# Performance work log

Measured on AMD Instinct MI355X. Metric: run time of the kernel, lower is better.

Reference implementation:

```python
import jax, jax.numpy as jnp
import numpy as np

B, T, LE = 8, 128, 128
V, VEXT = 32000, 32100
D, H, DFF, MAXLEN = 512, 8, 2048, 512


def _ln(x, g, b, eps=1e-5):
    m = jnp.mean(x, axis=-1, keepdims=True)
    v = jnp.mean((x - m) ** 2, axis=-1, keepdims=True)
    return (x - m) / jnp.sqrt(v + eps) * g + b


def _mha(q_in, k_in, v_in, in_w, in_b, out_w, out_b, mask=None):
    # torch nn.MultiheadAttention (batch_first): packed in_proj [3D, D]
    d = q_in.shape[-1]
    dh = d // H
    wq, wk, wv = in_w[:d], in_w[d:2 * d], in_w[2 * d:]
    bq, bk, bv = in_b[:d], in_b[d:2 * d], in_b[2 * d:]
    q = q_in @ wq.T + bq
    k = k_in @ wk.T + bk
    v = v_in @ wv.T + bv
    def split(x):  # [B, L, D] -> [B, H, L, dh]
        b, l, _ = x.shape
        return x.reshape(b, l, H, dh).transpose(0, 2, 1, 3)
    q, k, v = split(q), split(k), split(v)
    scores = jnp.einsum('bhqd,bhkd->bhqk', q, k) / jnp.sqrt(jnp.asarray(dh, q.dtype))
    if mask is not None:
        scores = scores + mask  # broadcast [T, T] additive mask
    attn = jax.nn.softmax(scores, axis=-1)  # [B, H, Lq, Lk]
    out = jnp.einsum('bhqk,bhkd->bhqd', attn, v)
    b, _, lq, _ = out.shape
    out = out.transpose(0, 2, 1, 3).reshape(b, lq, d)
    return out @ out_w.T + out_b, attn


def setup_inputs() -> dict:
    key = jax.random.key(0)
    ks = jax.random.split(key, 16)
    s = 0.02
    p = lambda i, shape: jax.random.normal(ks[i], shape, jnp.float32) * s
    return {
        'trg_input_ids': jax.random.randint(ks[0], (B, T), 0, V),
        'emofused': jax.random.normal(ks[1], (B, LE, D), jnp.float32),
        'src_token_ids': jax.random.randint(ks[2], (B, LE), 0, VEXT),
        'extended_vocab_size': VEXT,
        'tok_emb': p(3, (V, D)),
        'pos_emb': p(4, (MAXLEN, D)),
        'sa_in_w': p(5, (3 * D, D)), 'sa_in_b': jnp.zeros(3 * D, jnp.float32),
        'sa_out_w': p(6, (D, D)), 'sa_out_b': jnp.zeros(D, jnp.float32),
        'ca_in_w': p(7, (3 * D, D)), 'ca_in_b': jnp.zeros(3 * D, jnp.float32),
        'ca_out_w': p(8, (D, D)), 'ca_out_b': jnp.zeros(D, jnp.float32),
        'w1': p(9, (DFF, D)), 'b1': jnp.zeros(DFF, jnp.float32),
        'w2': p(10, (D, DFF)), 'b2': jnp.zeros(D, jnp.float32),
        'n1_g': jnp.ones(D, jnp.float32), 'n1_b': jnp.zeros(D, jnp.float32),
        'n2_g': jnp.ones(D, jnp.float32), 'n2_b': jnp.zeros(D, jnp.float32),
        'n3_g': jnp.ones(D, jnp.float32), 'n3_b': jnp.zeros(D, jnp.float32),
        'vp_w': p(11, (V, D)), 'vp_b': jnp.zeros(V, jnp.float32),
        'pg_w': p(12, (1, 3 * D)), 'pg_b': jnp.zeros(1, jnp.float32),
    }


def reference(trg_input_ids, emofused, src_token_ids, extended_vocab_size,
              tok_emb, pos_emb, sa_in_w, sa_in_b, sa_out_w, sa_out_b,
              ca_in_w, ca_in_b, ca_out_w, ca_out_b, w1, b1, w2, b2,
              n1_g, n1_b, n2_g, n2_b, n3_g, n3_b, vp_w, vp_b, pg_w, pg_b):
    t = trg_input_ids.shape[1]
    emb = tok_emb[trg_input_ids]                      # [B, T, D]
    x = emb + pos_emb[:t][None]
    # causal additive mask [T, T]
    idx = jnp.arange(t)
    mask = jnp.where(idx[None, :] > idx[:, None], jnp.asarray(-1e9, x.dtype), 0.0)
    # pre-norm self-attn
    h = _ln(x, n1_g, n1_b)
    sa, _ = _mha(h, h, h, sa_in_w, sa_in_b, sa_out_w, sa_out_b, mask)
    x = x + sa
    # pre-norm cross-attn (emofused is sole KV)
    h = _ln(x, n2_g, n2_b)
    ca, ca_attn = _mha(h, emofused, emofused, ca_in_w, ca_in_b, ca_out_w, ca_out_b)
    x = x + ca
    # FFN
    h = _ln(x, n3_g, n3_b)
    x = x + (jax.nn.relu(h @ w1.T + b1) @ w2.T + b2)
    hidden = x
    attn_avg = ca_attn.mean(axis=1)                   # [B, T, LE]
    ctx = jnp.einsum('btl,bld->btd', attn_avg, emofused)
    Pgen = jax.nn.softmax(hidden @ vp_w.T + vp_b, axis=-1)  # [B, T, V]
    gate_in = jnp.concatenate([hidden, ctx, emb], axis=-1)
    p_mix = jax.nn.sigmoid(gate_in @ pg_w.T + pg_b)   # [B, T, 1]
    vext = int(extended_vocab_size)
    def scat(aw, src):  # aw [T, LE], src [LE] -> [T, Vext]
        return jnp.zeros((aw.shape[0], vext), aw.dtype).at[:, src].add(aw)
    Pcopy = jax.vmap(scat)(attn_avg, src_token_ids)   # [B, T, Vext]
    Pgen_ext = jnp.pad(Pgen, ((0, 0), (0, 0), (0, vext - Pgen.shape[-1])))
    Pw = p_mix * Pgen_ext + (1.0 - p_mix) * Pcopy
    return Pw, Pgen_ext, Pcopy, p_mix, hidden, attn_avg, ctx
```

## Files before the change

### kernel.cpp

```cpp
#include <hip/hip_runtime.h>
#include <hip/hip_bf16.h>

using bf16   = __hip_bfloat16;
using bf16x8 = __attribute__((ext_vector_type(8))) __bf16;
using f32x4  = __attribute__((ext_vector_type(4))) float;
using short8 = __attribute__((ext_vector_type(8))) short;

__device__ __forceinline__ unsigned short f2b(float x) {
  union { bf16 b; unsigned short u; } t; t.b = __float2bfloat16(x); return t.u;
}

__global__ __launch_bounds__(256) void k_cast(const float* __restrict__ s, bf16* __restrict__ d, int n4) {
  int i = blockIdx.x * 256 + threadIdx.x;
  int str = gridDim.x * 256;
  for (; i < n4; i += str) {
    float4 v = ((const float4*)s)[i];
    ushort4 u; u.x = f2b(v.x); u.y = f2b(v.y); u.z = f2b(v.z); u.w = f2b(v.w);
    ((ushort4*)d)[i] = u;
  }
}

__global__ __launch_bounds__(128) void k_embed(const int* __restrict__ ids, const float* __restrict__ tok,
                                               const float* __restrict__ pos, float* __restrict__ x,
                                               float* __restrict__ emb) {
  int row = blockIdx.x;
  int tt  = row & 127;
  int id  = ids[row];
  int d   = threadIdx.x * 4;
  float4 e = *(const float4*)&tok[(size_t)id * 512 + d];
  float4 p = *(const float4*)&pos[(size_t)tt * 512 + d];
  *(float4*)&emb[(size_t)row * 512 + d] = e;
  float4 xv; xv.x = e.x + p.x; xv.y = e.y + p.y; xv.z = e.z + p.z; xv.w = e.w + p.w;
  *(float4*)&x[(size_t)row * 512 + d] = xv;
}

__global__ __launch_bounds__(256) void k_ln(const float* __restrict__ x, const float* __restrict__ g,
                                            const float* __restrict__ bb, bf16* __restrict__ o) {
  int wid = threadIdx.x >> 6, lane = threadIdx.x & 63;
  int row = blockIdx.x * 4 + wid;
  const float* xr = x + (size_t)row * 512;
  int d = lane * 8;
  float4 v0 = *(const float4*)&xr[d];
  float4 v1 = *(const float4*)&xr[d + 4];
  float s = v0.x + v0.y + v0.z + v0.w + v1.x + v1.y + v1.z + v1.w;
  float q = v0.x*v0.x + v0.y*v0.y + v0.z*v0.z + v0.w*v0.w
          + v1.x*v1.x + v1.y*v1.y + v1.z*v1.z + v1.w*v1.w;
#pragma unroll
  for (int t = 32; t; t >>= 1) { s += __shfl_xor(s, t); q += __shfl_xor(q, t); }
  float mean = s * (1.f / 512.f);
  float var  = q * (1.f / 512.f) - mean * mean;
  float rstd = rsqrtf(var + 1e-5f);
  float4 g0 = *(const float4*)&g[d],  g1 = *(const float4*)&g[d + 4];
  float4 b0 = *(const float4*)&bb[d], b1 = *(const float4*)&bb[d + 4];
  short8 pk;
  pk[0] = (short)f2b((v0.x - mean) * rstd * g0.x + b0.x);
  pk[1] = (short)f2b((v0.y - mean) * rstd * g0.y + b0.y);
  pk[2] = (short)f2b((v0.z - mean) * rstd * g0.z + b0.z);
  pk[3] = (short)f2b((v0.w - mean) * rstd * g0.w + b0.w);
  pk[4] = (short)f2b((v1.x - mean) * rstd * g1.x + b1.x);
  pk[5] = (short)f2b((v1.y - mean) * rstd * g1.y + b1.y);
  pk[6] = (short)f2b((v1.z - mean) * rstd * g1.z + b1.z);
  pk[7] = (short)f2b((v1.w - mean) * rstd * g1.w + b1.w);
  *(short8*)&o[(size_t)row * 512 + d] = pk;
}

template<int RELU, int RESID, int OUTBF>
__global__ __launch_bounds__(256) void k_gemm(const bf16* __restrict__ A, const bf16* __restrict__ Wt,
                                              const float* __restrict__ bias, const float* __restrict__ resid,
                                              void* __restrict__ Cout, int K, int ldc) {
  __shared__ unsigned short Al[128][48];
  __shared__ unsigned short Bl[128][48];
  int t = threadIdx.x;
  int lane = t & 63;
  int wid = t >> 6;
  int wr = wid >> 1, wc = wid & 1;
  int trow = blockIdx.y * 128, tcol = blockIdx.x * 128;
  f32x4 acc[4][4] = {};
  const int kh = (lane >> 4) * 8;
  const int rl = lane & 15;
  for (int kt = 0; kt < K; kt += 32) {
    __syncthreads();
#pragma unroll
    for (int s = 0; s < 2; ++s) {
      int chunk = t + s * 256;
      int row = chunk >> 2;
      int kc = (chunk & 3) * 8;
      *(short8*)&Al[row][kc] = *(const short8*)(A  + (size_t)(trow + row) * K + kt + kc);
      *(short8*)&Bl[row][kc] = *(const short8*)(Wt + (size_t)(tcol + row) * K + kt + kc);
    }
    __syncthreads();
    bf16x8 af[4], bg[4];
#pragma unroll
    for (int m = 0; m < 4; ++m) af[m] = *(const bf16x8*)&Al[wr * 64 + m * 16 + rl][kh];
#pragma unroll
    for (int n = 0; n < 4; ++n) bg[n] = *(const bf16x8*)&Bl[wc * 64 + n * 16 + rl][kh];
#pragma unroll
    for (int m = 0; m < 4; ++m)
#pragma unroll
      for (int n = 0; n < 4; ++n)
        acc[m][n] = __builtin_amdgcn_mfma_f32_16x16x32_bf16(af[m], bg[n], acc[m][n], 0, 0, 0);
  }
#pragma unroll
  for (int n = 0; n < 4; ++n) {
    int col = tcol + wc * 64 + n * 16 + rl;
    float bs = bias[col];
#pragma unroll
    for (int m = 0; m < 4; ++m) {
#pragma unroll
      for (int j = 0; j < 4; ++j) {
        int row = trow + wr * 64 + m * 16 + (lane >> 4) * 4 + j;
        float v = acc[m][n][j] + bs;
        if (RELU) v = fmaxf(v, 0.f);
        size_t idx = (size_t)row * ldc + col;
        if (RESID) v += resid[idx];
        if (OUTBF) ((bf16*)Cout)[idx] = __float2bfloat16(v);
        else       ((float*)Cout)[idx] = v;
      }
    }
  }
}

template<int MASK, int WPROB>
__global__ __launch_bounds__(256) void k_attn(const float* __restrict__ Qb, int qs,
                                              const float* __restrict__ Kb, int ks,
                                              const float* __restrict__ Vb, int vs,
                                              float* __restrict__ probs, bf16* __restrict__ Ob, int os) {
  __shared__ float KV[128][68];
  __shared__ float Sc[32][132];
  int t = threadIdx.x;
  int bh = blockIdx.x; int b = bh >> 3, h = bh & 7;
  int rb = blockIdx.y * 32;
  int r = t >> 3, sub = t & 7;
  const float* Kp = Kb + (size_t)(b * 128) * ks + h * 64;
  const float* Vp = Vb + (size_t)(b * 128) * vs + h * 64;
  const float* Qp = Qb + (size_t)(b * 128 + rb + r) * qs + h * 64;
  float4 q[16];
#pragma unroll
  for (int i = 0; i < 16; ++i) q[i] = *(const float4*)&Qp[i * 4];
  for (int i = 0; i < 32; ++i) { int u = t + i * 256; int rr = u >> 6, dd = u & 63; KV[rr][dd] = Kp[(size_t)rr * ks + dd]; }
  __syncthreads();
  float sc[16];
#pragma unroll
  for (int i = 0; i < 16; ++i) {
    int c = sub + i * 8;
    float a = 0.f;
#pragma unroll
    for (int d4 = 0; d4 < 16; ++d4) {
      float4 k4 = *(const float4*)&KV[c][d4 * 4];
      a += q[d4].x * k4.x + q[d4].y * k4.y + q[d4].z * k4.z + q[d4].w * k4.w;
    }
    a *= 0.125f;
    if (MASK && c > rb + r) a -= 1e9f;
    sc[i] = a;
  }
  float mx = -1e30f;
#pragma unroll
  for (int i = 0; i < 16; ++i) mx = fmaxf(mx, sc[i]);
  mx = fmaxf(mx, __shfl_xor(mx, 1)); mx = fmaxf(mx, __shfl_xor(mx, 2)); mx = fmaxf(mx, __shfl_xor(mx, 4));
  float sm = 0.f;
#pragma unroll
  for (int i = 0; i < 16; ++i) { sc[i] = __expf(sc[i] - mx); sm += sc[i]; }
  sm += __shfl_xor(sm, 1); sm += __shfl_xor(sm, 2); sm += __shfl_xor(sm, 4);
  float inv = 1.f / sm;
#pragma unroll
  for (int i = 0; i < 16; ++i) {
    float p = sc[i] * inv;
    Sc[r][sub + i * 8] = p;
    if (WPROB) probs[(((size_t)(b * 8 + h) * 128) + rb + r) * 128 + sub + i * 8] = p;
  }
  __syncthreads();
  for (int i = 0; i < 32; ++i) { int u = t + i * 256; int rr = u >> 6, dd = u & 63; KV[rr][dd] = Vp[(size_t)rr * vs + dd]; }
  __syncthreads();
  int dg = sub;
  float4 o0 = {0,0,0,0}, o1 = {0,0,0,0};
  for (int j = 0; j < 128; ++j) {
    float p = Sc[r][j];
    float4 va = *(const float4*)&KV[j][dg * 8];
    float4 vb = *(const float4*)&KV[j][dg * 8 + 4];
    o0.x += p * va.x; o0.y += p * va.y; o0.z += p * va.z; o0.w += p * va.w;
    o1.x += p * vb.x; o1.y += p * vb.y; o1.z += p * vb.z; o1.w += p * vb.w;
  }
  short8 pk;
  pk[0] = (short)f2b(o0.x); pk[1] = (short)f2b(o0.y); pk[2] = (short)f2b(o0.z); pk[3] = (short)f2b(o0.w);
  pk[4] = (short)f2b(o1.x); pk[5] = (short)f2b(o1.y); pk[6] = (short)f2b(o1.z); pk[7] = (short)f2b(o1.w);
  *(short8*)&Ob[(size_t)(b * 128 + rb + r) * os + h * 64 + dg * 8] = pk;
}

__global__ __launch_bounds__(256) void k_attn_avg(const float* __restrict__ abuf, float* __restrict__ aavg) {
  int e = blockIdx.x * 256 + threadIdx.x;
  int row = e >> 7, l = e & 127;
  int b = row >> 7, tt = row & 127;
  float s = 0.f;
#pragma unroll
  for (int h = 0; h < 8; ++h) s += abuf[(((size_t)(b * 8 + h) * 128) + tt) * 128 + l];
  aavg[e] = s * 0.125f;
}

__global__ __launch_bounds__(256) void k_ctx(const float* __restrict__ aavg, const float* __restrict__ emo,
                                             float* __restrict__ ctx) {
  __shared__ float aw[8][132];
  int b = blockIdx.x, rb = blockIdx.y * 8;
  int t = threadIdx.x;
  for (int i = t; i < 1024; i += 256) { int r = i >> 7, l = i & 127; aw[r][l] = aavg[(size_t)(b * 128 + rb + r) * 128 + l]; }
  __syncthreads();
  int d = t * 2;
  float2 acc[8] = {};
  for (int l = 0; l < 128; ++l) {
    float2 e = *(const float2*)&emo[(size_t)(b * 128 + l) * 512 + d];
#pragma unroll
    for (int r = 0; r < 8; ++r) { acc[r].x += aw[r][l] * e.x; acc[r].y += aw[r][l] * e.y; }
  }
#pragma unroll
  for (int r = 0; r < 8; ++r) *(float2*)&ctx[(size_t)(b * 128 + rb + r) * 512 + d] = acc[r];
}

__global__ __launch_bounds__(256) void k_hidden(const float* __restrict__ x, float* __restrict__ oh,
                                                bf16* __restrict__ hb) {
  int i = (blockIdx.x * 256 + threadIdx.x) * 4;
  float4 v = *(const float4*)&x[i];
  *(float4*)&oh[i] = v;
  ushort4 u; u.x = f2b(v.x); u.y = f2b(v.y); u.z = f2b(v.z); u.w = f2b(v.w);
  *(ushort4*)&hb[i] = u;
}

__global__ __launch_bounds__(256) void k_gate(const float* __restrict__ hid, const float* __restrict__ ctx,
                                              const float* __restrict__ emb, const float* __restrict__ pgw,
                                              const float* __restrict__ pgb, float* __restrict__ pmix) {
  int wid = threadIdx.x >> 6, lane = threadIdx.x & 63;
  int row = blockIdx.x * 4 + wid;
  float s = 0.f;
#pragma unroll
  for (int i = 0; i < 8; ++i) {
    int d = lane + i * 64;
    s = fmaf(hid[(size_t)row * 512 + d], pgw[d], s);
    s = fmaf(ctx[(size_t)row * 512 + d], pgw[512 + d], s);
    s = fmaf(emb[(size_t)row * 512 + d], pgw[1024 + d], s);
  }
#pragma unroll
  for (int t = 32; t; t >>= 1) s += __shfl_xor(s, t);
  if (lane == 0) pmix[row] = 1.f / (1.f + __expf(-(s + pgb[0])));
}

__global__ __launch_bounds__(256) void k_smstats(const float* __restrict__ lg, float* __restrict__ rm,
                                                 float* __restrict__ ri) {
  int row = blockIdx.x;
  const float4* L = (const float4*)(lg + (size_t)row * 32100);
  float m = -1e30f, s = 0.f;
  for (int i = threadIdx.x; i < 8000; i += 256) {
    float4 v = L[i];
    float vv[4] = {v.x, v.y, v.z, v.w};
#pragma unroll
    for (int c = 0; c < 4; ++c) {
      float xx = vv[c];
      if (xx > m) { s *= __expf(m - xx); m = xx; }
      s += __expf(xx - m);
    }
  }
#pragma unroll
  for (int o = 1; o < 64; o <<= 1) {
    float m2 = __shfl_xor(m, o), s2 = __shfl_xor(s, o);
    float M = fmaxf(m, m2);
    s = s * __expf(m - M) + s2 * __expf(m2 - M);
    m = M;
  }
  __shared__ float sm_[4], ss_[4];
  int wid = threadIdx.x >> 6, lane = threadIdx.x & 63;
  if (lane == 0) { sm_[wid] = m; ss_[wid] = s; }
  __syncthreads();
  if (threadIdx.x == 0) {
    m = sm_[0]; s = ss_[0];
#pragma unroll
    for (int w = 1; w < 4; ++w) {
      float M = fmaxf(m, sm_[w]);
      s = s * __expf(m - M) + ss_[w] * __expf(sm_[w] - M);
      m = M;
    }
    rm[row] = m; ri[row] = 1.f / s;
  }
}

__global__ __launch_bounds__(256) void k_final(float* __restrict__ pgen, float* __restrict__ pw,
                                               float* __restrict__ pcopy, const float* __restrict__ rm,
                                               const float* __restrict__ ri, const float* __restrict__ pmix) {
  int row = blockIdx.y;
  int c4 = blockIdx.x * 256 + threadIdx.x;
  if (c4 >= 8025) return;
  size_t base = (size_t)row * 8025 + c4;
  float4 o;
  if (c4 < 8000) {
    float m = rm[row], inv = ri[row];
    float4 L = ((const float4*)pgen)[base];
    o.x = __expf(L.x - m) * inv; o.y = __expf(L.y - m) * inv;
    o.z = __expf(L.z - m) * inv; o.w = __expf(L.w - m) * inv;
  } else { o.x = 0.f; o.y = 0.f; o.z = 0.f; o.w = 0.f; }
  ((float4*)pgen)[base] = o;
  float pm = pmix[row];
  float4 w; w.x = pm * o.x; w.y = pm * o.y; w.z = pm * o.z; w.w = pm * o.w;
  ((float4*)pw)[base] = w;
  float4 z; z.x = 0.f; z.y = 0.f; z.z = 0.f; z.w = 0.f;
  ((float4*)pcopy)[base] = z;
}

__global__ __launch_bounds__(256) void k_scatter(const int* __restrict__ src, const float* __restrict__ aavg,
                                                 const float* __restrict__ pmix, float* __restrict__ pw,
                                                 float* __restrict__ pcopy) {
  int tid = blockIdx.x * 256 + threadIdx.x;
  int row = tid >> 4, slot = tid & 15;
  int b = row >> 7;
  float qg = 1.f - pmix[row];
#pragma unroll
  for (int i = 0; i < 8; ++i) {
    int l = slot * 8 + i;
    int c = src[b * 128 + l];
    float w = aavg[(size_t)row * 128 + l];
    atomicAdd(&pcopy[(size_t)row * 32100 + c], w);
    atomicAdd(&pw[(size_t)row * 32100 + c], qg * w);
  }
}

extern "C" void kernel_launch(void* const* d_in, const int* in_sizes, int n_in,
                              void* d_out, int out_size, void* d_ws, size_t ws_size,
                              hipStream_t stream) {
  const int*   ids      = (const int*)d_in[0];
  const float* emo      = (const float*)d_in[1];
  const int*   src      = (const int*)d_in[2];
  const float* tok      = (const float*)d_in[4];
  const float* pos      = (const float*)d_in[5];
  const float* sa_in_w  = (const float*)d_in[6];
  const float* sa_in_b  = (const float*)d_in[7];
  const float* sa_out_w = (const float*)d_in[8];
  const float* sa_out_b = (const float*)d_in[9];
  const float* ca_in_w  = (const float*)d_in[10];
  const float* ca_in_b  = (const float*)d_in[11];
  const float* ca_out_w = (const float*)d_in[12];
  const float* ca_out_b = (const float*)d_in[13];
  const float* w1       = (const float*)d_in[14];
  const float* b1       = (const float*)d_in[15];
  const float* w2       = (const float*)d_in[16];
  const float* b2       = (const float*)d_in[17];
  const float* n1g      = (const float*)d_in[18];
  const float* n1b      = (const float*)d_in[19];
  const float* n2g      = (const float*)d_in[20];
  const float* n2b      = (const float*)d_in[21];
  const float* n3g      = (const float*)d_in[22];
  const float* n3b      = (const float*)d_in[23];
  const float* vpw      = (const float*)d_in[24];
  const float* vpb      = (const float*)d_in[25];
  const float* pgw      = (const float*)d_in[26];
  const float* pgb      = (const float*)d_in[27];
  (void)in_sizes; (void)n_in; (void)out_size; (void)ws_size;

  constexpr size_t NR = 1024;
  float* out     = (float*)d_out;
  float* o_pw    = out;
  float* o_pgen  = out + NR * 32100;
  float* o_pcopy = out + 2 * NR * 32100;
  float* o_pmix  = out + 3 * NR * 32100;
  float* o_hid   = o_pmix + NR;
  float* o_aavg  = o_hid + NR * 512;
  float* o_ctx   = o_aavg + NR * 128;

  char* w = (char*)d_ws;
  bf16* sa_in_bf  = (bf16*)(w + 0);
  bf16* sa_out_bf = (bf16*)(w + 1572864);
  bf16* ca_in_bf  = (bf16*)(w + 2097152);
  bf16* ca_out_bf = (bf16*)(w + 3670016);
  bf16* w1_bf     = (bf16*)(w + 4194304);
  bf16* w2_bf     = (bf16*)(w + 6291456);
  bf16* vp_bf     = (bf16*)(w + 8388608);
  bf16* emo_bf    = (bf16*)(w + 41156608);
  float* x        = (float*)(w + 42205184);
  float* embf     = (float*)(w + 44302336);
  bf16* hbf       = (bf16*)(w + 46399488);
  float* qkv      = (float*)(w + 47448064);
  bf16* aout_bf   = (bf16*)(w + 53739520);
  float* qca      = (float*)(w + 54788096);
  float* kvca     = (float*)(w + 56885248);
  float* abuf     = (float*)(w + 61079552);
  bf16* f1bf      = (bf16*)(w + 65273856);
  bf16* hid_bf    = (bf16*)(w + 69468160);
  float* rm       = (float*)(w + 70516736);
  float* ri       = (float*)(w + 70520832);

  k_cast<<<512, 256, 0, stream>>>(sa_in_w, sa_in_bf, 196608);
  k_cast<<<256, 256, 0, stream>>>(sa_out_w, sa_out_bf, 65536);
  k_cast<<<512, 256, 0, stream>>>(ca_in_w, ca_in_bf, 196608);
  k_cast<<<256, 256, 0, stream>>>(ca_out_w, ca_out_bf, 65536);
  k_cast<<<512, 256, 0, stream>>>(w1, w1_bf, 262144);
  k_cast<<<512, 256, 0, stream>>>(w2, w2_bf, 262144);
  k_cast<<<2048, 256, 0, stream>>>(vpw, vp_bf, 4096000);
  k_cast<<<512, 256, 0, stream>>>(emo, emo_bf, 131072);

  k_embed<<<1024, 128, 0, stream>>>(ids, tok, pos, x, embf);

  k_ln<<<256, 256, 0, stream>>>(x, n1g, n1b, hbf);
  k_gemm<0,0,0><<<dim3(12, 8), 256, 0, stream>>>(hbf, sa_in_bf, sa_in_b, nullptr, qkv, 512, 1536);
  k_attn<1,0><<<dim3(64, 4), 256, 0, stream>>>(qkv, 1536, qkv + 512, 1536, qkv + 1024, 1536,
                                               nullptr, aout_bf, 512);
  k_gemm<0,1,0><<<dim3(4, 8), 256, 0, stream>>>(aout_bf, sa_out_bf, sa_out_b, x, x, 512, 512);

  k_ln<<<256, 256, 0, stream>>>(x, n2g, n2b, hbf);
  k_gemm<0,0,0><<<dim3(4, 8), 256, 0, stream>>>(hbf, ca_in_bf, ca_in_b, nullptr, qca, 512, 512);
  k_gemm<0,0,0><<<dim3(8, 8), 256, 0, stream>>>(emo_bf, ca_in_bf + 512 * 512, ca_in_b + 512,
                                                nullptr, kvca, 512, 1024);
  k_attn<0,1><<<dim3(64, 4), 256, 0, stream>>>(qca, 512, kvca, 1024, kvca + 512, 1024,
                                               abuf, aout_bf, 512);
  k_attn_avg<<<512, 256, 0, stream>>>(abuf, o_aavg);
  k_gemm<0,1,0><<<dim3(4, 8), 256, 0, stream>>>(aout_bf, ca_out_bf, ca_out_b, x, x, 512, 512);

  k_ln<<<256, 256, 0, stream>>>(x, n3g, n3b, hbf);
  k_gemm<1,0,1><<<dim3(16, 8), 256, 0, stream>>>(hbf, w1_bf, b1, nullptr, f1bf, 512, 2048);
  k_gemm<0,1,0><<<dim3(4, 8), 256, 0, stream>>>(f1bf, w2_bf, b2, x, x, 2048, 512);

  k_hidden<<<512, 256, 0, stream>>>(x, o_hid, hid_bf);
  k_ctx<<<dim3(8, 16), 256, 0, stream>>>(o_aavg, emo, o_ctx);
  k_gate<<<256, 256, 0, stream>>>(o_hid, o_ctx, embf, pgw, pgb, o_pmix);

  k_gemm<0,0,0><<<dim3(250, 8), 256, 0, stream>>>(hid_bf, vp_bf, vpb, nullptr, o_pgen, 512, 32100);
  k_smstats<<<1024, 256, 0, stream>>>(o_pgen, rm, ri);
  k_final<<<dim3(32, 1024), 256, 0, stream>>>(o_pgen, o_pw, o_pcopy, rm, ri, o_pmix);
  k_scatter<<<64, 256, 0, stream>>>(src, o_aavg, o_pmix, o_pw, o_pcopy);
}
```

Before: 459.1 us.

## Stage vocab logits in bf16, fuse softmax, use direct LDS loads, batch casts

Several changes at once. The vocab GEMM now writes bf16 logits to a workspace buffer instead of fp32 into the output, and one row-per-block softmax kernel reads them three times and writes Pgen, Pw and Pcopy, replacing the separate stats and final kernels. The GEMM tile loads now go through global_load_lds straight into an unpadded LDS layout, and the seven small weight casts are merged into one launch. This cuts fp32 logit traffic and launch count. In exchange the logits are rounded to bf16 before the softmax, and the unpadded LDS may cause bank conflicts.

```diff
diff --git a/kernel.cpp b/kernel.cpp
--- a/kernel.cpp
+++ b/kernel.cpp
@@ -8,6 +8,15 @@
 
 __device__ __forceinline__ unsigned short f2b(float x) {
   union { bf16 b; unsigned short u; } t; t.b = __float2bfloat16(x); return t.u;
+}
+__device__ __forceinline__ float b2f(unsigned short u) {
+  union { unsigned int i; float f; } t; t.i = ((unsigned int)u) << 16; return t.f;
+}
+
+typedef __attribute__((address_space(1))) const unsigned int* gas1_t;
+typedef __attribute__((address_space(3))) unsigned int* las3_t;
+__device__ __forceinline__ void gload16(const void* g, void* l) {
+  __builtin_amdgcn_global_load_lds((gas1_t)g, (las3_t)l, 16, 0, 0);
 }
 
 __global__ __launch_bounds__(256) void k_cast(const float* __restrict__ s, bf16* __restrict__ d, int n4) {
@@ -18,6 +27,28 @@
     ushort4 u; u.x = f2b(v.x); u.y = f2b(v.y); u.z = f2b(v.z); u.w = f2b(v.w);
     ((ushort4*)d)[i] = u;
   }
+}
+
+__global__ __launch_bounds__(256) void k_cast_multi(
+    const float* __restrict__ s0, bf16* __restrict__ d0,
+    const float* __restrict__ s1, bf16* __restrict__ d1,
+    const float* __restrict__ s2, bf16* __restrict__ d2,
+    const float* __restrict__ s3, bf16* __restrict__ d3,
+    const float* __restrict__ s4, bf16* __restrict__ d4,
+    const float* __restrict__ s5, bf16* __restrict__ d5,
+    const float* __restrict__ s6, bf16* __restrict__ d6) {
+  int i = blockIdx.x * 256 + threadIdx.x;
+  const float* s; bf16* d; int off;
+  if      (i <  196608) { s = s0; d = d0; off = i; }
+  else if (i <  262144) { s = s1; d = d1; off = i - 196608; }
+  else if (i <  458752) { s = s2; d = d2; off = i - 262144; }
+  else if (i <  524288) { s = s3; d = d3; off = i - 458752; }
+  else if (i <  786432) { s = s4; d = d4; off = i - 524288; }
+  else if (i < 1048576) { s = s5; d = d5; off = i - 786432; }
+  else                  { s = s6; d = d6; off = i - 1048576; }
+  float4 v = ((const float4*)s)[off];
+  ushort4 u; u.x = f2b(v.x); u.y = f2b(v.y); u.z = f2b(v.z); u.w = f2b(v.w);
+  ((ushort4*)d)[off] = u;
 }
 
 __global__ __launch_bounds__(128) void k_embed(const int* __restrict__ ids, const float* __restrict__ tok,
@@ -68,8 +99,8 @@
 __global__ __launch_bounds__(256) void k_gemm(const bf16* __restrict__ A, const bf16* __restrict__ Wt,
                                               const float* __restrict__ bias, const float* __restrict__ resid,
                                               void* __restrict__ Cout, int K, int ldc) {
-  __shared__ unsigned short Al[128][48];
-  __shared__ unsigned short Bl[128][48];
+  __shared__ bf16 Al[128 * 32];
+  __shared__ bf16 Bl[128 * 32];
   int t = threadIdx.x;
   int lane = t & 63;
   int wid = t >> 6;
@@ -78,22 +109,23 @@
   f32x4 acc[4][4] = {};
   const int kh = (lane >> 4) * 8;
   const int rl = lane & 15;
+  const int srow = lane >> 2;
+  const int scol = (lane & 3) * 8;
   for (int kt = 0; kt < K; kt += 32) {
     __syncthreads();
 #pragma unroll
     for (int s = 0; s < 2; ++s) {
-      int chunk = t + s * 256;
-      int row = chunk >> 2;
-      int kc = (chunk & 3) * 8;
-      *(short8*)&Al[row][kc] = *(const short8*)(A  + (size_t)(trow + row) * K + kt + kc);
-      *(short8*)&Bl[row][kc] = *(const short8*)(Wt + (size_t)(tcol + row) * K + kt + kc);
+      int c = wid * 2 + s;
+      int row = c * 16 + srow;
+      gload16(A  + (size_t)(trow + row) * K + kt + scol, &Al[c * 512]);
+      gload16(Wt + (size_t)(tcol + row) * K + kt + scol, &Bl[c * 512]);
     }
     __syncthreads();
     bf16x8 af[4], bg[4];
 #pragma unroll
-    for (int m = 0; m < 4; ++m) af[m] = *(const bf16x8*)&Al[wr * 64 + m * 16 + rl][kh];
-#pragma unroll
-    for (int n = 0; n < 4; ++n) bg[n] = *(const bf16x8*)&Bl[wc * 64 + n * 16 + rl][kh];
+    for (int m = 0; m < 4; ++m) af[m] = *(const bf16x8*)&Al[(wr * 64 + m * 16 + rl) * 32 + kh];
+#pragma unroll
+    for (int n = 0; n < 4; ++n) bg[n] = *(const bf16x8*)&Bl[(wc * 64 + n * 16 + rl) * 32 + kh];
 #pragma unroll
     for (int m = 0; m < 4; ++m)
 #pragma unroll
@@ -241,64 +273,61 @@
   if (lane == 0) pmix[row] = 1.f / (1.f + __expf(-(s + pgb[0])));
 }
 
-__global__ __launch_bounds__(256) void k_smstats(const float* __restrict__ lg, float* __restrict__ rm,
-                                                 float* __restrict__ ri) {
+__global__ __launch_bounds__(256) void k_softmax_final(
+    const bf16* __restrict__ lg, const float* __restrict__ pmix,
+    float* __restrict__ pgen, float* __restrict__ pw, float* __restrict__ pcopy) {
+  __shared__ float red[8];
   int row = blockIdx.x;
-  const float4* L = (const float4*)(lg + (size_t)row * 32100);
-  float m = -1e30f, s = 0.f;
-  for (int i = threadIdx.x; i < 8000; i += 256) {
-    float4 v = L[i];
-    float vv[4] = {v.x, v.y, v.z, v.w};
-#pragma unroll
-    for (int c = 0; c < 4; ++c) {
-      float xx = vv[c];
-      if (xx > m) { s *= __expf(m - xx); m = xx; }
-      s += __expf(xx - m);
-    }
-  }
-#pragma unroll
-  for (int o = 1; o < 64; o <<= 1) {
-    float m2 = __shfl_xor(m, o), s2 = __shfl_xor(s, o);
-    float M = fmaxf(m, m2);
-    s = s * __expf(m - M) + s2 * __expf(m2 - M);
-    m = M;
-  }
-  __shared__ float sm_[4], ss_[4];
-  int wid = threadIdx.x >> 6, lane = threadIdx.x & 63;
-  if (lane == 0) { sm_[wid] = m; ss_[wid] = s; }
-  __syncthreads();
-  if (threadIdx.x == 0) {
-    m = sm_[0]; s = ss_[0];
-#pragma unroll
-    for (int w = 1; w < 4; ++w) {
-      float M = fmaxf(m, sm_[w]);
-      s = s * __expf(m - M) + ss_[w] * __expf(sm_[w] - M);
-      m = M;
-    }
-    rm[row] = m; ri[row] = 1.f / s;
-  }
-}
-
-__global__ __launch_bounds__(256) void k_final(float* __restrict__ pgen, float* __restrict__ pw,
-                                               float* __restrict__ pcopy, const float* __restrict__ rm,
-                                               const float* __restrict__ ri, const float* __restrict__ pmix) {
-  int row = blockIdx.y;
-  int c4 = blockIdx.x * 256 + threadIdx.x;
-  if (c4 >= 8025) return;
-  size_t base = (size_t)row * 8025 + c4;
-  float4 o;
-  if (c4 < 8000) {
-    float m = rm[row], inv = ri[row];
-    float4 L = ((const float4*)pgen)[base];
-    o.x = __expf(L.x - m) * inv; o.y = __expf(L.y - m) * inv;
-    o.z = __expf(L.z - m) * inv; o.w = __expf(L.w - m) * inv;
-  } else { o.x = 0.f; o.y = 0.f; o.z = 0.f; o.w = 0.f; }
-  ((float4*)pgen)[base] = o;
+  int t = threadIdx.x, lane = t & 63, wid = t >> 6;
+  const bf16* L = lg + (size_t)row * 32000;
+  float m = -1e30f;
+  for (int i = t; i < 4000; i += 256) {
+    short8 v = *(const short8*)(L + i * 8);
+#pragma unroll
+    for (int c = 0; c < 8; ++c) m = fmaxf(m, b2f((unsigned short)v[c]));
+  }
+#pragma unroll
+  for (int o = 32; o; o >>= 1) m = fmaxf(m, __shfl_xor(m, o));
+  if (lane == 0) red[wid] = m;
+  __syncthreads();
+  m = fmaxf(fmaxf(red[0], red[1]), fmaxf(red[2], red[3]));
+  float s = 0.f;
+  for (int i = t; i < 4000; i += 256) {
+    short8 v = *(const short8*)(L + i * 8);
+#pragma unroll
+    for (int c = 0; c < 8; ++c) s += __expf(b2f((unsigned short)v[c]) - m);
+  }
+#pragma unroll
+  for (int o = 32; o; o >>= 1) s += __shfl_xor(s, o);
+  if (lane == 0) red[4 + wid] = s;
+  __syncthreads();
+  s = red[4] + red[5] + red[6] + red[7];
+  float inv = 1.f / s;
   float pm = pmix[row];
-  float4 w; w.x = pm * o.x; w.y = pm * o.y; w.z = pm * o.z; w.w = pm * o.w;
-  ((float4*)pw)[base] = w;
-  float4 z; z.x = 0.f; z.y = 0.f; z.z = 0.f; z.w = 0.f;
-  ((float4*)pcopy)[base] = z;
+  float* pgen_r  = pgen  + (size_t)row * 32100;
+  float* pw_r    = pw    + (size_t)row * 32100;
+  float* pcopy_r = pcopy + (size_t)row * 32100;
+  float4 z = {0.f, 0.f, 0.f, 0.f};
+  for (int i = t; i < 4000; i += 256) {
+    short8 v = *(const short8*)(L + i * 8);
+    float p[8];
+#pragma unroll
+    for (int c = 0; c < 8; ++c) p[c] = __expf(b2f((unsigned short)v[c]) - m) * inv;
+    float4 a0 = {p[0], p[1], p[2], p[3]};
+    float4 a1 = {p[4], p[5], p[6], p[7]};
+    *(float4*)&pgen_r[i * 8]     = a0;
+    *(float4*)&pgen_r[i * 8 + 4] = a1;
+    float4 w0 = {pm * p[0], pm * p[1], pm * p[2], pm * p[3]};
+    float4 w1 = {pm * p[4], pm * p[5], pm * p[6], pm * p[7]};
+    *(float4*)&pw_r[i * 8]     = w0;
+    *(float4*)&pw_r[i * 8 + 4] = w1;
+    *(float4*)&pcopy_r[i * 8]     = z;
+    *(float4*)&pcopy_r[i * 8 + 4] = z;
+  }
+  if (t < 25) {
+    int c = 32000 + t * 4;
+    *(float4*)&pgen_r[c] = z; *(float4*)&pw_r[c] = z; *(float4*)&pcopy_r[c] = z;
+  }
 }
 
 __global__ __launch_bounds__(256) void k_scatter(const int* __restrict__ src, const float* __restrict__ aavg,
@@ -360,36 +389,33 @@
   float* o_aavg  = o_hid + NR * 512;
   float* o_ctx   = o_aavg + NR * 128;
 
-  char* w = (char*)d_ws;
-  bf16* sa_in_bf  = (bf16*)(w + 0);
-  bf16* sa_out_bf = (bf16*)(w + 1572864);
-  bf16* ca_in_bf  = (bf16*)(w + 2097152);
-  bf16* ca_out_bf = (bf16*)(w + 3670016);
-  bf16* w1_bf     = (bf16*)(w + 4194304);
-  bf16* w2_bf     = (bf16*)(w + 6291456);
-  bf16* vp_bf     = (bf16*)(w + 8388608);
-  bf16* emo_bf    = (bf16*)(w + 41156608);
-  float* x        = (float*)(w + 42205184);
-  float* embf     = (float*)(w + 44302336);
-  bf16* hbf       = (bf16*)(w + 46399488);
-  float* qkv      = (float*)(w + 47448064);
-  bf16* aout_bf   = (bf16*)(w + 53739520);
-  float* qca      = (float*)(w + 54788096);
-  float* kvca     = (float*)(w + 56885248);
-  float* abuf     = (float*)(w + 61079552);
-  bf16* f1bf      = (bf16*)(w + 65273856);
-  bf16* hid_bf    = (bf16*)(w + 69468160);
-  float* rm       = (float*)(w + 70516736);
-  float* ri       = (float*)(w + 70520832);
-
-  k_cast<<<512, 256, 0, stream>>>(sa_in_w, sa_in_bf, 196608);
-  k_cast<<<256, 256, 0, stream>>>(sa_out_w, sa_out_bf, 65536);
-  k_cast<<<512, 256, 0, stream>>>(ca_in_w, ca_in_bf, 196608);
-  k_cast<<<256, 256, 0, stream>>>(ca_out_w, ca_out_bf, 65536);
-  k_cast<<<512, 256, 0, stream>>>(w1, w1_bf, 262144);
-  k_cast<<<512, 256, 0, stream>>>(w2, w2_bf, 262144);
+  char* wp = (char*)d_ws;
+  size_t off = 0;
+  auto alloc = [&](size_t bytes) { char* r = wp + off; off += (bytes + 255) & ~(size_t)255; return r; };
+  bf16*  sa_in_bf  = (bf16*)alloc(3 * 512 * 512 * 2);
+  bf16*  sa_out_bf = (bf16*)alloc(512 * 512 * 2);
+  bf16*  ca_in_bf  = (bf16*)alloc(3 * 512 * 512 * 2);
+  bf16*  ca_out_bf = (bf16*)alloc(512 * 512 * 2);
+  bf16*  w1_bf     = (bf16*)alloc(2048 * 512 * 2);
+  bf16*  w2_bf     = (bf16*)alloc(2048 * 512 * 2);
+  bf16*  vp_bf     = (bf16*)alloc((size_t)32000 * 512 * 2);
+  bf16*  emo_bf    = (bf16*)alloc(8 * 128 * 512 * 2);
+  float* x         = (float*)alloc(1024 * 512 * 4);
+  float* embf      = (float*)alloc(1024 * 512 * 4);
+  bf16*  hbf       = (bf16*)alloc(1024 * 512 * 2);
+  float* qkv       = (float*)alloc(1024 * 1536 * 4);
+  bf16*  aout_bf   = (bf16*)alloc(1024 * 512 * 2);
+  float* qca       = (float*)alloc(1024 * 512 * 4);
+  float* kvca      = (float*)alloc(1024 * 1024 * 4);
+  float* abuf      = (float*)alloc((size_t)8 * 8 * 128 * 128 * 4);
+  bf16*  f1bf      = (bf16*)alloc(1024 * 2048 * 2);
+  bf16*  hid_bf    = (bf16*)alloc(1024 * 512 * 2);
+  bf16*  logits_bf = (bf16*)alloc((size_t)1024 * 32000 * 2);
+
+  k_cast_multi<<<4608, 256, 0, stream>>>(sa_in_w, sa_in_bf, sa_out_w, sa_out_bf,
+                                         ca_in_w, ca_in_bf, ca_out_w, ca_out_bf,
+                                         w1, w1_bf, w2, w2_bf, emo, emo_bf);
   k_cast<<<2048, 256, 0, stream>>>(vpw, vp_bf, 4096000);
-  k_cast<<<512, 256, 0, stream>>>(emo, emo_bf, 131072);
 
   k_embed<<<1024, 128, 0, stream>>>(ids, tok, pos, x, embf);
 
@@ -416,8 +442,7 @@
   k_ctx<<<dim3(8, 16), 256, 0, stream>>>(o_aavg, emo, o_ctx);
   k_gate<<<256, 256, 0, stream>>>(o_hid, o_ctx, embf, pgw, pgb, o_pmix);
 
-  k_gemm<0,0,0><<<dim3(250, 8), 256, 0, stream>>>(hid_bf, vp_bf, vpb, nullptr, o_pgen, 512, 32100);
-  k_smstats<<<1024, 256, 0, stream>>>(o_pgen, rm, ri);
-  k_final<<<dim3(32, 1024), 256, 0, stream>>>(o_pgen, o_pw, o_pcopy, rm, ri, o_pmix);
+  k_gemm<0,0,1><<<dim3(250, 8), 256, 0, stream>>>(hid_bf, vp_bf, vpb, nullptr, logits_bf, 512, 32000);
+  k_softmax_final<<<1024, 256, 0, stream>>>(logits_bf, o_pmix, o_pgen, o_pw, o_pcopy);
   k_scatter<<<64, 256, 0, stream>>>(src, o_aavg, o_pmix, o_pw, o_pcopy);
 }
```

After: 453.1 us. Within noise of the previous version (-1.3%).
